# Kernel optimization log

Hardware: AMD Instinct MI355X
Metric: run time of the kernel (lower is better)

The kernel has to match this reference:

```python
import jax, jax.numpy as jnp
import numpy as np

N = 100000   # nodes
E = 1600000  # edges
D = 128      # input feature dim
H = 128      # hidden dim
C = 40       # output classes


def _gcn_conv(x, W, b, src, dst, norm):
    # PyG GCNConv: h = x @ W; out_i = sum_j (d_i^-1/2 d_j^-1/2) h_j over in-edges,
    # including self-loops, then + bias. norm = deg^-1/2 with self-loop-augmented degree.
    h = x @ W                                    # [N, H]
    coef = norm[src] * norm[dst]                 # [E]
    agg = jax.ops.segment_sum(h[src] * coef[:, None], dst, num_segments=N)
    agg = agg + h * (norm * norm)[:, None]       # self-loop term
    return agg + b


def setup_inputs() -> dict:
    key = jax.random.key(0)
    ks = jax.random.split(key, 12)
    x = jax.random.normal(ks[0], (N, D), dtype=jnp.float32)
    edge_index = jax.random.randint(ks[1], (2, E), 0, N, dtype=jnp.int64)

    def lin(k, fan_in, fan_out):
        s = 1.0 / np.sqrt(fan_in)
        return jax.random.uniform(k, (fan_in, fan_out), jnp.float32, -s, s)

    return {
        "x": x,
        "edge_index": edge_index,
        "W1": lin(ks[2], D, H), "b1": jnp.zeros((H,), jnp.float32),
        "W2": lin(ks[3], H, H), "b2": jnp.zeros((H,), jnp.float32),
        "W3": lin(ks[4], H, H), "b3": jnp.zeros((H,), jnp.float32),
        "Wp1": lin(ks[5], H, H), "bp1": jnp.zeros((H,), jnp.float32),
        "Wp2": lin(ks[6], H, C), "bp2": jnp.zeros((C,), jnp.float32),
    }


def reference(x, edge_index, W1, b1, W2, b2, W3, b3, Wp1, bp1, Wp2, bp2):
    src, dst = edge_index[0], edge_index[1]
    # degree with self-loops (GCNConv adds self-loops by default)
    deg = jax.ops.segment_sum(jnp.ones((E,), jnp.float32), dst, num_segments=N) + 1.0
    norm = jax.lax.rsqrt(deg)                    # deg^-1/2

    h = x
    for W, b in ((W1, b1), (W2, b2), (W3, b3)):
        h = _gcn_conv(h, W, b, src, dst, norm)
        h = jax.nn.relu(h)
        # dropout is a no-op at inference / rate 0

    h = h @ Wp1 + bp1
    h = h @ Wp2 + bp2
    return jax.nn.log_softmax(h, axis=1)
```

## Files before the change

kernel.cpp:

```cpp
#include <hip/hip_runtime.h>
#include <hip/hip_bf16.h>
#include <math.h>


#define DH 128
#define NC 40
#define BN 128
#define MAXNB 1024
#define CAP 2560
#define CH 4096
#define SP 136

typedef __attribute__((ext_vector_type(8))) short bf16x8;
typedef __attribute__((ext_vector_type(4))) float f32x4;

__device__ __forceinline__ unsigned short f2bf(float f) {
    unsigned u = __float_as_uint(f);
    unsigned r = (u + 0x7fffu + ((u >> 16) & 1u)) >> 16;
    return (unsigned short)r;
}
__device__ __forceinline__ unsigned pack2(float lo, float hi) {
    return (unsigned)f2bf(lo) | ((unsigned)f2bf(hi) << 16);
}


__global__ __launch_bounds__(256) void init_bpos(unsigned* __restrict__ bpos, int NB) {
    int i = blockIdx.x * 256 + threadIdx.x;
    if (i < NB) bpos[i] = (unsigned)i * CAP;
}


__global__ __launch_bounds__(256) void bucket_scatter(const int* __restrict__ src,
                                                      const int* __restrict__ dst, int E,
                                                      unsigned* __restrict__ bpos,
                                                      unsigned* __restrict__ ebuf) {
    __shared__ unsigned hist[MAXNB];
    __shared__ unsigned gbase[MAXNB];
    __shared__ unsigned lim[MAXNB];
    __shared__ unsigned cur[MAXNB];
    int tid = threadIdx.x;
    int e0 = blockIdx.x * CH;
    int nE = min(CH, E - e0);
    int nE4 = nE & ~3;

    for (int i = tid; i < MAXNB; i += 256) { hist[i] = 0; cur[i] = 0; }
    __syncthreads();
    for (int i = tid * 4; i < nE4; i += 1024) {
        int4 dv = *(const int4*)(dst + e0 + i);
        atomicAdd(&hist[(unsigned)dv.x >> 7], 1u);
        atomicAdd(&hist[(unsigned)dv.y >> 7], 1u);
        atomicAdd(&hist[(unsigned)dv.z >> 7], 1u);
        atomicAdd(&hist[(unsigned)dv.w >> 7], 1u);
    }
    for (int i = nE4 + tid; i < nE; i += 256)
        atomicAdd(&hist[(unsigned)dst[e0 + i] >> 7], 1u);
    __syncthreads();
    for (int i = tid; i < MAXNB; i += 256) {
        unsigned h = hist[i];
        if (h) {
            unsigned o = atomicAdd(&bpos[i], h);
            gbase[i] = o;
            lim[i] = min(o + h, (unsigned)(i + 1) * CAP);
        }
    }
    __syncthreads();
    for (int i = tid * 4; i < nE4; i += 1024) {
        int4 sv = *(const int4*)(src + e0 + i);
        int4 dv = *(const int4*)(dst + e0 + i);
        {
            unsigned b = (unsigned)dv.x >> 7;
            unsigned p = gbase[b] + atomicAdd(&cur[b], 1u);
            if (p < lim[b]) ebuf[p] = ((unsigned)sv.x << 7) | ((unsigned)dv.x & 127u);
        }
        {
            unsigned b = (unsigned)dv.y >> 7;
            unsigned p = gbase[b] + atomicAdd(&cur[b], 1u);
            if (p < lim[b]) ebuf[p] = ((unsigned)sv.y << 7) | ((unsigned)dv.y & 127u);
        }
        {
            unsigned b = (unsigned)dv.z >> 7;
            unsigned p = gbase[b] + atomicAdd(&cur[b], 1u);
            if (p < lim[b]) ebuf[p] = ((unsigned)sv.z << 7) | ((unsigned)dv.z & 127u);
        }
        {
            unsigned b = (unsigned)dv.w >> 7;
            unsigned p = gbase[b] + atomicAdd(&cur[b], 1u);
            if (p < lim[b]) ebuf[p] = ((unsigned)sv.w << 7) | ((unsigned)dv.w & 127u);
        }
    }
    for (int i = nE4 + tid; i < nE; i += 256) {
        int s = src[e0 + i];
        int d = dst[e0 + i];
        unsigned b = (unsigned)d >> 7;
        unsigned p = gbase[b] + atomicAdd(&cur[b], 1u);
        if (p < lim[b]) ebuf[p] = ((unsigned)s << 7) | ((unsigned)d & 127u);
    }
}


__global__ __launch_bounds__(256) void bucket_degfill(const unsigned* __restrict__ ebuf,
                                                      const unsigned* __restrict__ bpos,
                                                      unsigned* __restrict__ cnt,
                                                      float* __restrict__ nrm,
                                                      unsigned* __restrict__ offN,
                                                      unsigned* __restrict__ dh,
                                                      int* __restrict__ csr, int N) {
    __shared__ unsigned h[BN], lb[BN], cur[BN];
    __shared__ int lcsr[CAP];
    __shared__ unsigned dhh[256];
    __shared__ unsigned tot;

    int b = blockIdx.x, tid = threadIdx.x;
    unsigned ebase = (unsigned)b * CAP;
    unsigned used = min(bpos[b] - ebase, (unsigned)CAP);
    unsigned used4 = used & ~3u;

    if (tid < BN) { h[tid] = 0; cur[tid] = 0; }
    dhh[tid] = 0;
    if (tid == 0) tot = 0;
    __syncthreads();

    for (unsigned i = tid * 4; i < used4; i += 1024) {
        uint4 v = *(const uint4*)(ebuf + ebase + i);
        atomicAdd(&h[v.x & 127u], 1u);
        atomicAdd(&h[v.y & 127u], 1u);
        atomicAdd(&h[v.z & 127u], 1u);
        atomicAdd(&h[v.w & 127u], 1u);
    }
    for (unsigned i = used4 + tid; i < used; i += 256)
        atomicAdd(&h[ebuf[ebase + i] & 127u], 1u);
    __syncthreads();

    if (tid < BN) {
        unsigned m = h[tid];
        lb[tid] = m ? atomicAdd(&tot, m) : 0u;
    }
    __syncthreads();

    for (unsigned i = tid * 4; i < used4; i += 1024) {
        uint4 v = *(const uint4*)(ebuf + ebase + i);
        {
            unsigned nl = v.x & 127u;
            unsigned r = atomicAdd(&cur[nl], 1u);
            lcsr[lb[nl] + r] = (int)(v.x >> 7);
        }
        {
            unsigned nl = v.y & 127u;
            unsigned r = atomicAdd(&cur[nl], 1u);
            lcsr[lb[nl] + r] = (int)(v.y >> 7);
        }
        {
            unsigned nl = v.z & 127u;
            unsigned r = atomicAdd(&cur[nl], 1u);
            lcsr[lb[nl] + r] = (int)(v.z >> 7);
        }
        {
            unsigned nl = v.w & 127u;
            unsigned r = atomicAdd(&cur[nl], 1u);
            lcsr[lb[nl] + r] = (int)(v.w >> 7);
        }
    }
    for (unsigned i = used4 + tid; i < used; i += 256) {
        unsigned v = ebuf[ebase + i];
        unsigned nl = v & 127u;
        unsigned r = atomicAdd(&cur[nl], 1u);
        lcsr[lb[nl] + r] = (int)(v >> 7);
    }

    if (tid < BN) {
        int node = b * BN + tid;
        if (node < N) {
            unsigned m = h[tid];
            cnt[node] = m;
            nrm[node] = rsqrtf((float)m + 1.0f);
            offN[node] = ebase + lb[tid];
            atomicAdd(&dhh[min(m, 255u)], 1u);
        }
    }
    __syncthreads();

    for (unsigned i = tid * 4; i < used4; i += 1024)
        *(int4*)(csr + ebase + i) = *(const int4*)&lcsr[i];
    for (unsigned i = used4 + tid; i < used; i += 256)
        csr[ebase + i] = lcsr[i];
    if (dhh[tid]) atomicAdd(&dh[tid], dhh[tid]);
}


__global__ __launch_bounds__(256) void deg_scatter(const unsigned* __restrict__ cnt, int N,
                                                   const unsigned* __restrict__ dh,
                                                   unsigned* __restrict__ binpos,
                                                   const unsigned* __restrict__ offN,
                                                   int* __restrict__ perm,
                                                   unsigned* __restrict__ pd2) {
    __shared__ unsigned hh[256], base[256], cur[256], sdh[256], sns[256];
    int t = threadIdx.x;
    hh[t] = 0; cur[t] = 0; sdh[t] = dh[t];
    __syncthreads();
    unsigned ns = 0;
    for (int d = t + 1; d < 256; ++d) ns += sdh[d];
    sns[t] = ns;
    int i = blockIdx.x * 256 + t;
    unsigned d = 0;
    if (i < N) { d = min(cnt[i], 255u); atomicAdd(&hh[d], 1u); }
    __syncthreads();
    if (hh[t]) base[t] = sns[t] + atomicAdd(&binpos[t], hh[t]);
    __syncthreads();
    if (i < N) {
        unsigned r = atomicAdd(&cur[d], 1u);
        unsigned idx = base[d] + r;
        perm[idx] = i;
        pd2[idx] = (offN[i] << 9) | min(cnt[i], 511u);
    }
}


__global__ __launch_bounds__(256) void prep_w(const float* __restrict__ W1,
                                              const float* __restrict__ W2,
                                              const float* __restrict__ W3,
                                              const float* __restrict__ Wp1,
                                              const float* __restrict__ bp1,
                                              const float* __restrict__ Wp2,
                                              const float* __restrict__ bp2,
                                              unsigned short* __restrict__ Wt,
                                              unsigned short* __restrict__ Wft,
                                              float* __restrict__ bfh) {
    int id = blockIdx.x * 256 + threadIdx.x;
    if (id < 3 * DH * DH) {
        int l = id >> 14, r = id & (DH * DH - 1);
        int k = r >> 7, n = r & 127;
        const float* W = (l == 0) ? W1 : (l == 1) ? W2 : W3;
        Wt[l * DH * DH + n * DH + k] = f2bf(W[k * DH + n]);
    } else if (id < 3 * DH * DH + 48 * DH) {
        int o = id - 3 * DH * DH;
        int c = o >> 7, k = o & 127;
        float acc = 0.f;
        if (c < NC)
            for (int j = 0; j < DH; ++j) acc += Wp1[k * DH + j] * Wp2[j * NC + c];
        Wft[c * DH + k] = f2bf(acc);
    } else if (id < 3 * DH * DH + 48 * DH + 48) {
        int c = id - 3 * DH * DH - 48 * DH;
        float acc = 0.f;
        if (c < NC) {
            acc = bp2[c];
            for (int j = 0; j < DH; ++j) acc += bp1[j] * Wp2[j * NC + c];
        }
        bfh[c] = acc;
    }
}


__global__ __launch_bounds__(256) void gemm_mfma_f32(const float* __restrict__ X,
                                                     const unsigned short* __restrict__ Wt,
                                                     const float* __restrict__ nrm,
                                                     unsigned short* __restrict__ outb,
                                                     int nrows) {
    const int tid = threadIdx.x;
    const int wave = tid >> 6;
    const int lane = tid & 63;
    const int m = lane & 15;
    const int quad = lane >> 4;
    const int rbase = blockIdx.x * 128 + wave * 32;

    union U8 { bf16x8 v; unsigned u[4]; };

    f32x4 acc[2][8];
#pragma unroll
    for (int rt = 0; rt < 2; ++rt)
#pragma unroll
        for (int ct = 0; ct < 8; ++ct) acc[rt][ct] = (f32x4){0.f, 0.f, 0.f, 0.f};

#pragma unroll
    for (int kt = 0; kt < 4; ++kt) {
        const int kof = kt * 32 + quad * 8;
        bf16x8 a[2], b[8];
#pragma unroll
        for (int rt = 0; rt < 2; ++rt) {
            int r = rbase + rt * 16 + m;
            r = (r < nrows) ? r : (nrows - 1);
            const float* p = X + (size_t)r * DH + kof;
            float4 u0 = *(const float4*)p;
            float4 u1 = *(const float4*)(p + 4);
            U8 t;
            t.u[0] = pack2(u0.x, u0.y);
            t.u[1] = pack2(u0.z, u0.w);
            t.u[2] = pack2(u1.x, u1.y);
            t.u[3] = pack2(u1.z, u1.w);
            a[rt] = t.v;
        }
#pragma unroll
        for (int ct = 0; ct < 8; ++ct)
            b[ct] = *(const bf16x8*)(Wt + (ct * 16 + m) * DH + kof);
#pragma unroll
        for (int rt = 0; rt < 2; ++rt)
#pragma unroll
            for (int ct = 0; ct < 8; ++ct)
                acc[rt][ct] = __builtin_amdgcn_mfma_f32_16x16x32_bf16(a[rt], b[ct], acc[rt][ct], 0, 0, 0);
    }

#pragma unroll
    for (int rt = 0; rt < 2; ++rt)
#pragma unroll
        for (int reg = 0; reg < 4; ++reg) {
            int r = rbase + rt * 16 + quad * 4 + reg;
            if (r < nrows) {
                float s = nrm[r];
#pragma unroll
                for (int ct = 0; ct < 8; ++ct)
                    outb[(size_t)r * DH + ct * 16 + m] = f2bf(acc[rt][ct][reg] * s);
            }
        }
}


__device__ __forceinline__ void bf8_add(float* acc, uint4 v) {
    acc[0] += __uint_as_float(v.x << 16);
    acc[1] += __uint_as_float(v.x & 0xffff0000u);
    acc[2] += __uint_as_float(v.y << 16);
    acc[3] += __uint_as_float(v.y & 0xffff0000u);
    acc[4] += __uint_as_float(v.z << 16);
    acc[5] += __uint_as_float(v.z & 0xffff0000u);
    acc[6] += __uint_as_float(v.w << 16);
    acc[7] += __uint_as_float(v.w & 0xffff0000u);
}

__device__ __forceinline__ void gather_phase(const uint4* __restrict__ Abf,
                                             const int* __restrict__ csr,
                                             const unsigned* __restrict__ pd2,
                                             const int* __restrict__ perm,
                                             const float* __restrict__ bias,
                                             unsigned short (*sA)[SP],
                                             int* snode, float* snrm, int N) {
    const int tid = threadIdx.x;
    const int g = tid >> 4;
    const int lane = tid & 15;
    const int idx = blockIdx.x * 16 + g;
    if (idx < N) {
        const unsigned pd = pd2[idx];
        const unsigned o = pd >> 9;
        const unsigned d = pd & 511u;
        const int node = perm[idx];

        int i0 = 0, i1 = 0, i2 = 0, i3 = 0;
        if ((unsigned)lane < d)      i0 = csr[o + lane];
        if ((unsigned)(16 + lane) < d) i1 = csr[o + 16 + lane];
        if ((unsigned)(32 + lane) < d) i2 = csr[o + 32 + lane];
        if ((unsigned)(48 + lane) < d) i3 = csr[o + 48 + lane];

        float acc[8];
        {
            uint4 v = Abf[(size_t)node * 16 + lane];
            acc[0] = __uint_as_float(v.x << 16);
            acc[1] = __uint_as_float(v.x & 0xffff0000u);
            acc[2] = __uint_as_float(v.y << 16);
            acc[3] = __uint_as_float(v.y & 0xffff0000u);
            acc[4] = __uint_as_float(v.z << 16);
            acc[5] = __uint_as_float(v.z & 0xffff0000u);
            acc[6] = __uint_as_float(v.w << 16);
            acc[7] = __uint_as_float(v.w & 0xffff0000u);
        }

        const unsigned dl = min(d, 64u);
        const int sb = g << 4;
        unsigned e = 0;
        for (; e + 4 <= dl; e += 4) {
            int rsel = (e < 16) ? i0 : (e < 32) ? i1 : (e < 48) ? i2 : i3;
            int bb = sb + (int)(e & 15u);
            int s0 = __shfl(rsel, bb + 0);
            int s1 = __shfl(rsel, bb + 1);
            int s2 = __shfl(rsel, bb + 2);
            int s3 = __shfl(rsel, bb + 3);
            uint4 v0 = Abf[(size_t)s0 * 16 + lane];
            uint4 v1 = Abf[(size_t)s1 * 16 + lane];
            uint4 v2 = Abf[(size_t)s2 * 16 + lane];
            uint4 v3 = Abf[(size_t)s3 * 16 + lane];
            bf8_add(acc, v0);
            bf8_add(acc, v1);
            bf8_add(acc, v2);
            bf8_add(acc, v3);
        }
        for (; e < dl; ++e) {
            int rsel = (e < 16) ? i0 : (e < 32) ? i1 : (e < 48) ? i2 : i3;
            int s = __shfl(rsel, sb + (int)(e & 15u));
            uint4 v = Abf[(size_t)s * 16 + lane];
            bf8_add(acc, v);
        }
        for (; e < d; ++e) {
            int s = csr[o + e];
            uint4 v = Abf[(size_t)s * 16 + lane];
            bf8_add(acc, v);
        }

        float nm = rsqrtf((float)d + 1.0f);
        if (lane == 0) { snode[g] = node; snrm[g] = nm; }
        float4 b0 = *(const float4*)(bias + lane * 8);
        float4 b1 = *(const float4*)(bias + lane * 8 + 4);
        uint4 ov;
        ov.x = pack2(fmaxf(acc[0] * nm + b0.x, 0.f), fmaxf(acc[1] * nm + b0.y, 0.f));
        ov.y = pack2(fmaxf(acc[2] * nm + b0.z, 0.f), fmaxf(acc[3] * nm + b0.w, 0.f));
        ov.z = pack2(fmaxf(acc[4] * nm + b1.x, 0.f), fmaxf(acc[5] * nm + b1.y, 0.f));
        ov.w = pack2(fmaxf(acc[6] * nm + b1.z, 0.f), fmaxf(acc[7] * nm + b1.w, 0.f));
        *(uint4*)&sA[g][lane * 8] = ov;
    }
    __syncthreads();
}


__global__ __launch_bounds__(256, 8) void agg_gemm(const uint4* __restrict__ Abf,
                                                   const int* __restrict__ csr,
                                                   const unsigned* __restrict__ pd2,
                                                   const int* __restrict__ perm,
                                                   const float* __restrict__ bias,
                                                   const unsigned short* __restrict__ Wt,
                                                   unsigned short* __restrict__ outb, int N) {
    __shared__ unsigned short sA[16][SP];
    __shared__ int snode[16];
    __shared__ float snrm[16];
    gather_phase(Abf, csr, pd2, perm, bias, sA, snode, snrm, N);

    const int tid = threadIdx.x;
    const int wave = tid >> 6;
    const int l64 = tid & 63;
    const int m = l64 & 15;
    const int quad = l64 >> 4;

    f32x4 acc[2];
    acc[0] = (f32x4){0.f, 0.f, 0.f, 0.f};
    acc[1] = (f32x4){0.f, 0.f, 0.f, 0.f};

#pragma unroll
    for (int kt = 0; kt < 4; ++kt) {
        const int kof = kt * 32 + quad * 8;
        bf16x8 a = *(const bf16x8*)&sA[m][kof];
#pragma unroll
        for (int c2 = 0; c2 < 2; ++c2) {
            const int ct = wave * 2 + c2;
            bf16x8 b = *(const bf16x8*)(Wt + (ct * 16 + m) * DH + kof);
            acc[c2] = __builtin_amdgcn_mfma_f32_16x16x32_bf16(a, b, acc[c2], 0, 0, 0);
        }
    }

#pragma unroll
    for (int reg = 0; reg < 4; ++reg) {
        int idx = blockIdx.x * 16 + quad * 4 + reg;
        if (idx < N) {
            int r = snode[quad * 4 + reg];
            float s = snrm[quad * 4 + reg];
#pragma unroll
            for (int c2 = 0; c2 < 2; ++c2)
                outb[(size_t)r * DH + (wave * 2 + c2) * 16 + m] = f2bf(acc[c2][reg] * s);
        }
    }
}


__global__ __launch_bounds__(256, 8) void agg_head(const uint4* __restrict__ Abf,
                                                   const int* __restrict__ csr,
                                                   const unsigned* __restrict__ pd2,
                                                   const int* __restrict__ perm,
                                                   const float* __restrict__ bias,
                                                   const unsigned short* __restrict__ Wft,
                                                   const float* __restrict__ bfh,
                                                   float* __restrict__ out, int N) {
    __shared__ unsigned short sA[16][SP];
    __shared__ int snode[16];
    __shared__ float snrm[16];
    gather_phase(Abf, csr, pd2, perm, bias, sA, snode, snrm, N);

    const int tid = threadIdx.x;
    if (tid >= 64) return;
    const int m = tid & 15;
    const int quad = tid >> 4;

    f32x4 acc[3];
#pragma unroll
    for (int ct = 0; ct < 3; ++ct) acc[ct] = (f32x4){0.f, 0.f, 0.f, 0.f};

#pragma unroll
    for (int kt = 0; kt < 4; ++kt) {
        const int kof = kt * 32 + quad * 8;
        bf16x8 a = *(const bf16x8*)&sA[m][kof];
#pragma unroll
        for (int ct = 0; ct < 3; ++ct) {
            bf16x8 b = *(const bf16x8*)(Wft + (ct * 16 + m) * DH + kof);
            acc[ct] = __builtin_amdgcn_mfma_f32_16x16x32_bf16(a, b, acc[ct], 0, 0, 0);
        }
    }

    float bias0 = bfh[m];
    float bias1 = bfh[16 + m];
    float bias2 = bfh[32 + m];

#pragma unroll
    for (int reg = 0; reg < 4; ++reg) {
        float v0 = acc[0][reg] + bias0;
        float v1 = acc[1][reg] + bias1;
        float v2 = (m < 8) ? (acc[2][reg] + bias2) : -1e30f;
        float mx = fmaxf(fmaxf(v0, v1), v2);
#pragma unroll
        for (int dlt = 1; dlt < 16; dlt <<= 1) mx = fmaxf(mx, __shfl_xor(mx, dlt));
        float s = __expf(v0 - mx) + __expf(v1 - mx) + ((m < 8) ? __expf(v2 - mx) : 0.f);
#pragma unroll
        for (int dlt = 1; dlt < 16; dlt <<= 1) s += __shfl_xor(s, dlt);
        float ls = mx + __logf(s);
        int idx = blockIdx.x * 16 + quad * 4 + reg;
        if (idx < N) {
            int r = snode[quad * 4 + reg];
            out[(size_t)r * NC + m] = v0 - ls;
            out[(size_t)r * NC + 16 + m] = v1 - ls;
            if (m < 8) out[(size_t)r * NC + 32 + m] = v2 - ls;
        }
    }
}


extern "C" void kernel_launch(void* const* d_in, const int* in_sizes, int n_in,
                              void* d_out, int out_size, void* d_ws, size_t ws_size,
                              hipStream_t stream) {
    const float* x   = (const float*)d_in[0];
    const int*   ei  = (const int*)d_in[1];
    const float* W1  = (const float*)d_in[2];
    const float* b1  = (const float*)d_in[3];
    const float* W2  = (const float*)d_in[4];
    const float* b2  = (const float*)d_in[5];
    const float* W3  = (const float*)d_in[6];
    const float* b3  = (const float*)d_in[7];
    const float* Wp1 = (const float*)d_in[8];
    const float* bp1 = (const float*)d_in[9];
    const float* Wp2 = (const float*)d_in[10];
    const float* bp2 = (const float*)d_in[11];
    float* out = (float*)d_out;

    const int N = in_sizes[0] / DH;
    const int E = in_sizes[1] / 2;
    const int* src = ei;
    const int* dst = ei + E;
    const int NB = (N + BN - 1) / BN;

    char* w = (char*)d_ws;
    unsigned short* Ab  = (unsigned short*)w; w += (size_t)N * DH * 2;
    unsigned short* Bb  = (unsigned short*)w; w += (size_t)N * DH * 2;
    int*      csr    = (int*)w;      w += (size_t)NB * CAP * 4;
    unsigned* ebuf   = (unsigned*)w; w += (size_t)NB * CAP * 4;
    unsigned* dh     = (unsigned*)w; w += 256 * 4;
    unsigned* binpos = (unsigned*)w; w += 256 * 4;
    unsigned* bpos   = (unsigned*)w; w += MAXNB * 4;
    unsigned* cnt    = (unsigned*)w; w += (size_t)N * 4;
    float*    nrm    = (float*)w;    w += (size_t)N * 4;
    unsigned* offN   = (unsigned*)w; w += (size_t)N * 4;
    unsigned* pd2    = (unsigned*)w; w += (size_t)((N + 31) & ~31) * 4;
    int*      perm   = (int*)w;      w += (size_t)((N + 31) & ~31) * 4;
    unsigned short* Wt  = (unsigned short*)w; w += 3 * DH * DH * 2;
    unsigned short* Wft = (unsigned short*)w; w += 48 * DH * 2;
    float*    bfh    = (float*)w;    w += 64 * 4;

    const int gC = (E + CH - 1) / CH;
    const int gN = (N + 255) / 256;

    hipMemsetAsync(dh, 0, 256 * 4 + 256 * 4, stream);
    init_bpos     <<<(NB + 255) / 256, 256, 0, stream>>>(bpos, NB);
    bucket_scatter<<<gC, 256, 0, stream>>>(src, dst, E, bpos, ebuf);
    bucket_degfill<<<NB, 256, 0, stream>>>(ebuf, bpos, cnt, nrm, offN, dh, csr, N);
    deg_scatter   <<<gN, 256, 0, stream>>>(cnt, N, dh, binpos, offN, perm, pd2);
    prep_w<<<(3 * DH * DH + 48 * DH + 48 + 255) / 256, 256, 0, stream>>>(
        W1, W2, W3, Wp1, bp1, Wp2, bp2, Wt, Wft, bfh);

    const int gG = (N + 127) / 128;
    const int gF = (N + 15) / 16;

    gemm_mfma_f32<<<gG, 256, 0, stream>>>(x, Wt, nrm, Ab, N);
    agg_gemm<<<gF, 256, 0, stream>>>((const uint4*)Ab, csr, pd2, perm, b1,
                                     Wt + DH * DH, Bb, N);
    agg_gemm<<<gF, 256, 0, stream>>>((const uint4*)Bb, csr, pd2, perm, b2,
                                     Wt + 2 * DH * DH, Ab, N);
    agg_head<<<gF, 256, 0, stream>>>((const uint4*)Ab, csr, pd2, perm, b3,
                                     Wft, bfh, out, N);
}
```

Measured before the change: 380.1 us.

## Stage bucket scatter in LDS and double-buffer gather loads

The bucket scatter kernel now reads each edge once into registers, builds a locally bucket-sorted copy in shared memory, and writes it out in coalesced runs. This replaces the second global read of src/dst and the scattered global stores. The gather loop in the aggregation kernels is software-pipelined with two register sets of four rows, so the next group's loads are issued before the current group is accumulated. Launch bounds drop from 8 to 6 blocks per CU to leave room for the extra registers, which may lower occupancy.

```diff
diff --git a/kernel.cpp b/kernel.cpp
--- a/kernel.cpp
+++ b/kernel.cpp
@@ -34,66 +34,90 @@
                                                       const int* __restrict__ dst, int E,
                                                       unsigned* __restrict__ bpos,
                                                       unsigned* __restrict__ ebuf) {
+    __shared__ unsigned word[CH];
+    __shared__ unsigned short sbkt[CH];
     __shared__ unsigned hist[MAXNB];
-    __shared__ unsigned gbase[MAXNB];
-    __shared__ unsigned lim[MAXNB];
+    __shared__ unsigned gb[MAXNB];
+    __shared__ unsigned lb[MAXNB];
     __shared__ unsigned cur[MAXNB];
-    int tid = threadIdx.x;
-    int e0 = blockIdx.x * CH;
-    int nE = min(CH, E - e0);
-    int nE4 = nE & ~3;
+    __shared__ unsigned tot;
+
+    const int tid = threadIdx.x;
+    const int e0 = blockIdx.x * CH;
+    const int nE = min(CH, E - e0);
 
     for (int i = tid; i < MAXNB; i += 256) { hist[i] = 0; cur[i] = 0; }
-    __syncthreads();
-    for (int i = tid * 4; i < nE4; i += 1024) {
-        int4 dv = *(const int4*)(dst + e0 + i);
-        atomicAdd(&hist[(unsigned)dv.x >> 7], 1u);
-        atomicAdd(&hist[(unsigned)dv.y >> 7], 1u);
-        atomicAdd(&hist[(unsigned)dv.z >> 7], 1u);
-        atomicAdd(&hist[(unsigned)dv.w >> 7], 1u);
-    }
-    for (int i = nE4 + tid; i < nE; i += 256)
-        atomicAdd(&hist[(unsigned)dst[e0 + i] >> 7], 1u);
-    __syncthreads();
+    if (tid == 0) tot = 0;
+    __syncthreads();
+
+    unsigned wr[16];
+    unsigned short br[16];
+
+#pragma unroll
+    for (int q = 0; q < 4; ++q) {
+        const int i = q * 1024 + tid * 4;
+        if (i + 3 < nE) {
+            int4 sv = *(const int4*)(src + e0 + i);
+            int4 dv = *(const int4*)(dst + e0 + i);
+            wr[q * 4 + 0] = ((unsigned)sv.x << 7) | ((unsigned)dv.x & 127u);
+            wr[q * 4 + 1] = ((unsigned)sv.y << 7) | ((unsigned)dv.y & 127u);
+            wr[q * 4 + 2] = ((unsigned)sv.z << 7) | ((unsigned)dv.z & 127u);
+            wr[q * 4 + 3] = ((unsigned)sv.w << 7) | ((unsigned)dv.w & 127u);
+            br[q * 4 + 0] = (unsigned short)((unsigned)dv.x >> 7);
+            br[q * 4 + 1] = (unsigned short)((unsigned)dv.y >> 7);
+            br[q * 4 + 2] = (unsigned short)((unsigned)dv.z >> 7);
+            br[q * 4 + 3] = (unsigned short)((unsigned)dv.w >> 7);
+            atomicAdd(&hist[br[q * 4 + 0]], 1u);
+            atomicAdd(&hist[br[q * 4 + 1]], 1u);
+            atomicAdd(&hist[br[q * 4 + 2]], 1u);
+            atomicAdd(&hist[br[q * 4 + 3]], 1u);
+        } else {
+#pragma unroll
+            for (int k = 0; k < 4; ++k) {
+                if (i + k < nE) {
+                    int s = src[e0 + i + k];
+                    int d = dst[e0 + i + k];
+                    wr[q * 4 + k] = ((unsigned)s << 7) | ((unsigned)d & 127u);
+                    br[q * 4 + k] = (unsigned short)((unsigned)d >> 7);
+                    atomicAdd(&hist[br[q * 4 + k]], 1u);
+                } else {
+                    wr[q * 4 + k] = 0u;
+                    br[q * 4 + k] = 0;
+                }
+            }
+        }
+    }
+    __syncthreads();
+
     for (int i = tid; i < MAXNB; i += 256) {
         unsigned h = hist[i];
         if (h) {
-            unsigned o = atomicAdd(&bpos[i], h);
-            gbase[i] = o;
-            lim[i] = min(o + h, (unsigned)(i + 1) * CAP);
-        }
-    }
-    __syncthreads();
-    for (int i = tid * 4; i < nE4; i += 1024) {
-        int4 sv = *(const int4*)(src + e0 + i);
-        int4 dv = *(const int4*)(dst + e0 + i);
-        {
-            unsigned b = (unsigned)dv.x >> 7;
-            unsigned p = gbase[b] + atomicAdd(&cur[b], 1u);
-            if (p < lim[b]) ebuf[p] = ((unsigned)sv.x << 7) | ((unsigned)dv.x & 127u);
-        }
-        {
-            unsigned b = (unsigned)dv.y >> 7;
-            unsigned p = gbase[b] + atomicAdd(&cur[b], 1u);
-            if (p < lim[b]) ebuf[p] = ((unsigned)sv.y << 7) | ((unsigned)dv.y & 127u);
-        }
-        {
-            unsigned b = (unsigned)dv.z >> 7;
-            unsigned p = gbase[b] + atomicAdd(&cur[b], 1u);
-            if (p < lim[b]) ebuf[p] = ((unsigned)sv.z << 7) | ((unsigned)dv.z & 127u);
-        }
-        {
-            unsigned b = (unsigned)dv.w >> 7;
-            unsigned p = gbase[b] + atomicAdd(&cur[b], 1u);
-            if (p < lim[b]) ebuf[p] = ((unsigned)sv.w << 7) | ((unsigned)dv.w & 127u);
-        }
-    }
-    for (int i = nE4 + tid; i < nE; i += 256) {
-        int s = src[e0 + i];
-        int d = dst[e0 + i];
-        unsigned b = (unsigned)d >> 7;
-        unsigned p = gbase[b] + atomicAdd(&cur[b], 1u);
-        if (p < lim[b]) ebuf[p] = ((unsigned)s << 7) | ((unsigned)d & 127u);
+            lb[i] = atomicAdd(&tot, h);
+            gb[i] = atomicAdd(&bpos[i], h);
+        }
+    }
+    __syncthreads();
+
+#pragma unroll
+    for (int q = 0; q < 4; ++q) {
+#pragma unroll
+        for (int k = 0; k < 4; ++k) {
+            const int i = q * 1024 + tid * 4 + k;
+            if (i < nE) {
+                unsigned b = br[q * 4 + k];
+                unsigned r = atomicAdd(&cur[b], 1u);
+                unsigned p = lb[b] + r;
+                word[p] = wr[q * 4 + k];
+                sbkt[p] = (unsigned short)b;
+            }
+        }
+    }
+    __syncthreads();
+
+    for (int p = tid; p < nE; p += 256) {
+        unsigned b = sbkt[p];
+        unsigned pg = gb[b] + ((unsigned)p - lb[b]);
+        if (pg < (unsigned)(b + 1) * CAP) ebuf[pg] = word[p];
     }
 }
 
@@ -324,6 +348,21 @@
     acc[7] += __uint_as_float(v.w & 0xffff0000u);
 }
 
+#define GLOAD(B0, B1, B2, B3, base_)                                            \
+    {                                                                           \
+        unsigned bb_ = (base_);                                                 \
+        int rsel_ = (bb_ < 16) ? i0 : (bb_ < 32) ? i1 : (bb_ < 48) ? i2 : i3;   \
+        int lb_ = sb + (int)(bb_ & 15u);                                        \
+        int t0_ = __shfl(rsel_, lb_ + 0);                                       \
+        int t1_ = __shfl(rsel_, lb_ + 1);                                       \
+        int t2_ = __shfl(rsel_, lb_ + 2);                                       \
+        int t3_ = __shfl(rsel_, lb_ + 3);                                       \
+        B0 = Abf[(size_t)t0_ * 16 + lane];                                      \
+        B1 = Abf[(size_t)t1_ * 16 + lane];                                      \
+        B2 = Abf[(size_t)t2_ * 16 + lane];                                      \
+        B3 = Abf[(size_t)t3_ * 16 + lane];                                      \
+    }
+
 __device__ __forceinline__ void gather_phase(const uint4* __restrict__ Abf,
                                              const int* __restrict__ csr,
                                              const unsigned* __restrict__ pd2,
@@ -342,7 +381,7 @@
         const int node = perm[idx];
 
         int i0 = 0, i1 = 0, i2 = 0, i3 = 0;
-        if ((unsigned)lane < d)      i0 = csr[o + lane];
+        if ((unsigned)lane < d)        i0 = csr[o + lane];
         if ((unsigned)(16 + lane) < d) i1 = csr[o + 16 + lane];
         if ((unsigned)(32 + lane) < d) i2 = csr[o + 32 + lane];
         if ((unsigned)(48 + lane) < d) i3 = csr[o + 48 + lane];
@@ -362,22 +401,31 @@
 
         const unsigned dl = min(d, 64u);
         const int sb = g << 4;
+        const unsigned nb = dl >> 2;
         unsigned e = 0;
-        for (; e + 4 <= dl; e += 4) {
-            int rsel = (e < 16) ? i0 : (e < 32) ? i1 : (e < 48) ? i2 : i3;
-            int bb = sb + (int)(e & 15u);
-            int s0 = __shfl(rsel, bb + 0);
-            int s1 = __shfl(rsel, bb + 1);
-            int s2 = __shfl(rsel, bb + 2);
-            int s3 = __shfl(rsel, bb + 3);
-            uint4 v0 = Abf[(size_t)s0 * 16 + lane];
-            uint4 v1 = Abf[(size_t)s1 * 16 + lane];
-            uint4 v2 = Abf[(size_t)s2 * 16 + lane];
-            uint4 v3 = Abf[(size_t)s3 * 16 + lane];
-            bf8_add(acc, v0);
-            bf8_add(acc, v1);
-            bf8_add(acc, v2);
-            bf8_add(acc, v3);
+        if (nb) {
+            uint4 va0, va1, va2, va3, vb0, vb1, vb2, vb3;
+            GLOAD(va0, va1, va2, va3, 0u);
+            unsigned k = 1;
+            for (; k + 1 < nb; k += 2) {
+                GLOAD(vb0, vb1, vb2, vb3, k * 4u);
+                bf8_add(acc, va0); bf8_add(acc, va1);
+                bf8_add(acc, va2); bf8_add(acc, va3);
+                GLOAD(va0, va1, va2, va3, (k + 1) * 4u);
+                bf8_add(acc, vb0); bf8_add(acc, vb1);
+                bf8_add(acc, vb2); bf8_add(acc, vb3);
+            }
+            if (k < nb) {
+                GLOAD(vb0, vb1, vb2, vb3, k * 4u);
+                bf8_add(acc, va0); bf8_add(acc, va1);
+                bf8_add(acc, va2); bf8_add(acc, va3);
+                bf8_add(acc, vb0); bf8_add(acc, vb1);
+                bf8_add(acc, vb2); bf8_add(acc, vb3);
+            } else {
+                bf8_add(acc, va0); bf8_add(acc, va1);
+                bf8_add(acc, va2); bf8_add(acc, va3);
+            }
+            e = nb * 4u;
         }
         for (; e < dl; ++e) {
             int rsel = (e < 16) ? i0 : (e < 32) ? i1 : (e < 48) ? i2 : i3;
@@ -406,7 +454,7 @@
 }
 
 
-__global__ __launch_bounds__(256, 8) void agg_gemm(const uint4* __restrict__ Abf,
+__global__ __launch_bounds__(256, 6) void agg_gemm(const uint4* __restrict__ Abf,
                                                    const int* __restrict__ csr,
                                                    const unsigned* __restrict__ pd2,
                                                    const int* __restrict__ perm,
@@ -454,7 +502,7 @@
 }
 
 
-__global__ __launch_bounds__(256, 8) void agg_head(const uint4* __restrict__ Abf,
+__global__ __launch_bounds__(256, 6) void agg_head(const uint4* __restrict__ Abf,
                                                    const int* __restrict__ csr,
                                                    const unsigned* __restrict__ pd2,
                                                    const int* __restrict__ perm,
```

Result: slower. 390.4 us (+2.7%).
